# Performance work log

Hardware: AMD Instinct MI355X
Metric: run time of the kernel (lower is better)

The kernel has to match this reference:

```python
import jax, jax.numpy as jnp
import numpy as np

B, H, W, C = 32, 256, 256, 3
KH, KW, F = 5, 5, 8


def setup_inputs() -> dict:
    key = jax.random.key(0)
    k1, k2 = jax.random.split(key)
    x = jax.random.normal(k1, (B, H, W, C), dtype=jnp.float32)
    # learned structuring elements, shape (KH, KW, C, F) per build()
    kernel = jax.random.normal(k2, (KH, KW, C, F), dtype=jnp.float32) * 0.1
    return {"x": x, "kernel": kernel}


def _max_of_erosions(x, kernel):
    # tf.nn.erosion2d semantics: out[b,y,x,c] = min_{dy,dx} in[b, y+dy-pt, x+dx-pl, c]
    #                                               - kernel[KH-1-dy, KW-1-dx, c]
    # (erosion = -dilation(-x, reversed kernel)); then channel-max per filter.
    Bq, Hq, Wq, Cq = x.shape
    kh, kw, _, nf = kernel.shape
    pad_h, pad_w = kh - 1, kw - 1          # stride 1, rate 1, SAME padding
    pt, pl = pad_h // 2, pad_w // 2
    xp = jnp.pad(x, ((0, 0), (pt, pad_h - pt), (pl, pad_w - pl), (0, 0)),
                 constant_values=jnp.inf)   # +inf is identity for min
    kflip = kernel[::-1, ::-1]              # reflected structuring element
    ero = None                              # running min over window taps
    for dy in range(kh):                    # small fixed 5x5 tap loop
        for dx in range(kw):
            win = xp[:, dy:dy + Hq, dx:dx + Wq, :]          # [B,H,W,C]
            cand = win[..., None] - kflip[dy, dx]           # [B,H,W,C,F]
            ero = cand if ero is None else jnp.minimum(ero, cand)
    return jnp.max(ero, axis=3)             # channel max -> [B,H,W,F]


def reference(x, kernel):
    return _max_of_erosions(x, kernel)
```

## Files before the change

kernel.cpp:

```cpp
#include <hip/hip_runtime.h>
#include <math.h>


typedef _Float16 h2 __attribute__((ext_vector_type(2)));

static __device__ __forceinline__ h2 cvt_pk(float a, float b) {
    return __builtin_bit_cast(h2, __builtin_amdgcn_cvt_pkrtz(a, b));
}

#define Bq 32
#define Hq 256
#define Wq 256
#define Cq 3
#define NF 8

__global__ __launch_bounds__(256) void maxero_f16(
    const float* __restrict__ x,
    const float* __restrict__ kern,
    float* __restrict__ out)
{
    __shared__ h2 klds[25 * 12];
    for (int i = threadIdx.x; i < 300; i += 256) {
        int tap = i / 12;
        int rem = i - tap * 12;
        int c  = rem >> 2;
        int fp = rem & 3;
        int dy = tap / 5, dx = tap - dy * 5;
        const float* kp = kern + (((4 - dy) * 5 + (4 - dx)) * (Cq * NF)) + c * NF + fp * 2;
        klds[i] = cvt_pk(kp[0], kp[1]);
    }
    __syncthreads();

    const int idx  = blockIdx.x * 256 + threadIdx.x;
    const int pix0 = idx * 4;
    const int w0 = pix0 & (Wq - 1);
    const int h  = (pix0 >> 8) & (Hq - 1);
    const int b  = pix0 >> 16;

    const _Float16 HINF = (_Float16)__builtin_huge_valf();
    const h2 inf2 = { HINF, HINF };

    h2 ero[4][3][4];
    #pragma unroll
    for (int p = 0; p < 4; ++p)
        #pragma unroll
        for (int c = 0; c < 3; ++c)
            #pragma unroll
            for (int fp = 0; fp < 4; ++fp)
                ero[p][c][fp] = inf2;

    const float* xb = x + (size_t)b * (Hq * Wq * Cq);

    #pragma unroll
    for (int dy = 0; dy < 5; ++dy) {
        int r = h + dy - 2;
        bool rin = (unsigned)r < (unsigned)Hq;
        int rc = min(max(r, 0), Hq - 1);
        const float* rowp = xb + rc * (Wq * Cq);

        h2 xq[8][3];
        #pragma unroll
        for (int j = 0; j < 8; ++j) {
            int ccol = w0 - 2 + j;
            bool vin = rin && ((unsigned)ccol < (unsigned)Wq);
            int ccl = min(max(ccol, 0), Wq - 1);
            const float* p = rowp + ccl * 3;
            float v0 = p[0], v1 = p[1], v2 = p[2];
            h2 t0 = cvt_pk(v0, v0);
            h2 t1 = cvt_pk(v1, v1);
            h2 t2 = cvt_pk(v2, v2);
            xq[j][0] = vin ? t0 : inf2;
            xq[j][1] = vin ? t1 : inf2;
            xq[j][2] = vin ? t2 : inf2;
        }

        #pragma unroll
        for (int dx = 0; dx < 5; ++dx) {
            const h2* kk = &klds[(dy * 5 + dx) * 12];
            h2 kr[12];
            #pragma unroll
            for (int t = 0; t < 12; ++t) kr[t] = kk[t];
            #pragma unroll
            for (int p = 0; p < 4; ++p) {
                #pragma unroll
                for (int c = 0; c < 3; ++c) {
                    #pragma unroll
                    for (int fp = 0; fp < 4; ++fp) {
                        h2 cand = xq[p + dx][c] - kr[c * 4 + fp];
                        ero[p][c][fp] = __builtin_elementwise_min(ero[p][c][fp], cand);
                    }
                }
            }
        }
    }

    #pragma unroll
    for (int p = 0; p < 4; ++p) {
        float of[8];
        #pragma unroll
        for (int fp = 0; fp < 4; ++fp) {
            h2 m = __builtin_elementwise_max(
                       __builtin_elementwise_max(ero[p][0][fp], ero[p][1][fp]),
                       ero[p][2][fp]);
            of[fp * 2 + 0] = (float)m[0];
            of[fp * 2 + 1] = (float)m[1];
        }
        float* op = out + (size_t)(pix0 + p) * NF;
        reinterpret_cast<float4*>(op)[0] = make_float4(of[0], of[1], of[2], of[3]);
        reinterpret_cast<float4*>(op)[1] = make_float4(of[4], of[5], of[6], of[7]);
    }
}

extern "C" void kernel_launch(void* const* d_in, const int* in_sizes, int n_in,
                              void* d_out, int out_size, void* d_ws, size_t ws_size,
                              hipStream_t stream) {
    const float* x    = (const float*)d_in[0];
    const float* kern = (const float*)d_in[1];
    float* out        = (float*)d_out;
    const int threads = (Bq * Hq * Wq) / 4;
    maxero_f16<<<threads / 256, 256, 0, stream>>>(x, kern, out);
}
```

Baseline: 57.70 us.

## Stage input halo tile in LDS as packed f16 and read via vector loads

Each block now covers 4 output rows of one image. It loads the 8-row halo tile cooperatively with float4 global loads, converts it to packed f16 once, and stores it in LDS with inf padding. Threads then read their window rows as 128-bit LDS loads instead of issuing many scalar, clamped global loads and conversions per tap row. Kernel taps are also read as uint4. This trades the redundant global traffic and per-thread conversion work for LDS use (about 25KB per block) and a barrier, which may limit occupancy.

```diff
diff --git a/kernel.cpp b/kernel.cpp
--- a/kernel.cpp
+++ b/kernel.cpp
@@ -7,38 +7,66 @@
 static __device__ __forceinline__ h2 cvt_pk(float a, float b) {
     return __builtin_bit_cast(h2, __builtin_amdgcn_cvt_pkrtz(a, b));
 }
+static __device__ __forceinline__ h2 u2h(unsigned u) {
+    return __builtin_bit_cast(h2, u);
+}
 
 #define Bq 32
 #define Hq 256
 #define Wq 256
-#define Cq 3
-#define NF 8
 
-__global__ __launch_bounds__(256) void maxero_f16(
+#define RSTR 792
+#define TILE_H2 (8 * RSTR)
+
+#define INF2 0x7C007C00u
+
+__global__ __launch_bounds__(256) void maxero_lds(
     const float* __restrict__ x,
     const float* __restrict__ kern,
     float* __restrict__ out)
 {
+    __shared__ h2 xlds[TILE_H2];
     __shared__ h2 klds[25 * 12];
-    for (int i = threadIdx.x; i < 300; i += 256) {
+
+    const int tid = threadIdx.x;
+    const int bI  = blockIdx.x;
+    const int b   = bI >> 6;
+    const int h0  = (bI & 63) << 2;
+
+    for (int i = tid; i < 300; i += 256) {
         int tap = i / 12;
         int rem = i - tap * 12;
-        int c  = rem >> 2;
-        int fp = rem & 3;
+        int c = rem >> 2, fp = rem & 3;
         int dy = tap / 5, dx = tap - dy * 5;
-        const float* kp = kern + (((4 - dy) * 5 + (4 - dx)) * (Cq * NF)) + c * NF + fp * 2;
+        const float* kp = kern + (((4 - dy) * 5 + (4 - dx)) * 24) + c * 8 + fp * 2;
         klds[i] = cvt_pk(kp[0], kp[1]);
+    }
+
+    const float* xb = x + (size_t)b * (Hq * Wq * 3);
+    #pragma unroll
+    for (int k = 0; k < 6; ++k) {
+        int chunk = tid + k * 256;
+        int rr    = chunk / 192;
+        int off   = (chunk - rr * 192) * 4;
+        int r     = h0 - 2 + rr;
+        bool rv   = (unsigned)r < (unsigned)Hq;
+        int rc    = min(max(r, 0), Hq - 1);
+        const float4 v = *reinterpret_cast<const float4*>(xb + rc * 768 + off);
+        h2* d = &xlds[rr * RSTR + 18 + off];
+        d[0] = rv ? cvt_pk(v.x, v.x) : u2h(INF2);
+        d[1] = rv ? cvt_pk(v.y, v.y) : u2h(INF2);
+        d[2] = rv ? cvt_pk(v.z, v.z) : u2h(INF2);
+        d[3] = rv ? cvt_pk(v.w, v.w) : u2h(INF2);
+    }
+    if (tid < 192) {
+        int rr = tid / 24, p = tid - rr * 24;
+        int idx = rr * RSTR + (p < 18 ? p : 768 + p);
+        xlds[idx] = u2h(INF2);
     }
     __syncthreads();
 
-    const int idx  = blockIdx.x * 256 + threadIdx.x;
-    const int pix0 = idx * 4;
-    const int w0 = pix0 & (Wq - 1);
-    const int h  = (pix0 >> 8) & (Hq - 1);
-    const int b  = pix0 >> 16;
-
-    const _Float16 HINF = (_Float16)__builtin_huge_valf();
-    const h2 inf2 = { HINF, HINF };
+    const int hrow = tid >> 6;
+    const int w0   = (tid & 63) << 2;
 
     h2 ero[4][3][4];
     #pragma unroll
@@ -47,50 +75,32 @@
         for (int c = 0; c < 3; ++c)
             #pragma unroll
             for (int fp = 0; fp < 4; ++fp)
-                ero[p][c][fp] = inf2;
-
-    const float* xb = x + (size_t)b * (Hq * Wq * Cq);
+                ero[p][c][fp] = u2h(INF2);
 
     #pragma unroll
     for (int dy = 0; dy < 5; ++dy) {
-        int r = h + dy - 2;
-        bool rin = (unsigned)r < (unsigned)Hq;
-        int rc = min(max(r, 0), Hq - 1);
-        const float* rowp = xb + rc * (Wq * Cq);
-
-        h2 xq[8][3];
-        #pragma unroll
-        for (int j = 0; j < 8; ++j) {
-            int ccol = w0 - 2 + j;
-            bool vin = rin && ((unsigned)ccol < (unsigned)Wq);
-            int ccl = min(max(ccol, 0), Wq - 1);
-            const float* p = rowp + ccl * 3;
-            float v0 = p[0], v1 = p[1], v2 = p[2];
-            h2 t0 = cvt_pk(v0, v0);
-            h2 t1 = cvt_pk(v1, v1);
-            h2 t2 = cvt_pk(v2, v2);
-            xq[j][0] = vin ? t0 : inf2;
-            xq[j][1] = vin ? t1 : inf2;
-            xq[j][2] = vin ? t2 : inf2;
-        }
-
+        const uint4* rp = reinterpret_cast<const uint4*>(
+            &xlds[(hrow + dy) * RSTR + 12 + 3 * w0]);
+        uint4 q0 = rp[0], q1 = rp[1], q2 = rp[2], q3 = rp[3], q4 = rp[4], q5 = rp[5];
+        const unsigned qf[24] = { q0.x,q0.y,q0.z,q0.w, q1.x,q1.y,q1.z,q1.w,
+                                  q2.x,q2.y,q2.z,q2.w, q3.x,q3.y,q3.z,q3.w,
+                                  q4.x,q4.y,q4.z,q4.w, q5.x,q5.y,q5.z,q5.w };
         #pragma unroll
         for (int dx = 0; dx < 5; ++dx) {
-            const h2* kk = &klds[(dy * 5 + dx) * 12];
-            h2 kr[12];
+            const uint4* kk = reinterpret_cast<const uint4*>(&klds[(dy * 5 + dx) * 12]);
+            uint4 k0 = kk[0], k1 = kk[1], k2 = kk[2];
+            const unsigned kf[12] = { k0.x,k0.y,k0.z,k0.w,
+                                      k1.x,k1.y,k1.z,k1.w,
+                                      k2.x,k2.y,k2.z,k2.w };
             #pragma unroll
-            for (int t = 0; t < 12; ++t) kr[t] = kk[t];
-            #pragma unroll
-            for (int p = 0; p < 4; ++p) {
+            for (int p = 0; p < 4; ++p)
                 #pragma unroll
-                for (int c = 0; c < 3; ++c) {
+                for (int c = 0; c < 3; ++c)
                     #pragma unroll
                     for (int fp = 0; fp < 4; ++fp) {
-                        h2 cand = xq[p + dx][c] - kr[c * 4 + fp];
+                        h2 cand = u2h(qf[(p + dx) * 3 + c]) - u2h(kf[c * 4 + fp]);
                         ero[p][c][fp] = __builtin_elementwise_min(ero[p][c][fp], cand);
                     }
-                }
-            }
         }
     }
 
@@ -105,7 +115,8 @@
             of[fp * 2 + 0] = (float)m[0];
             of[fp * 2 + 1] = (float)m[1];
         }
-        float* op = out + (size_t)(pix0 + p) * NF;
+        size_t opix = ((size_t)b * 65536 + (size_t)(h0 + hrow) * 256 + (w0 + p));
+        float* op = out + opix * 8;
         reinterpret_cast<float4*>(op)[0] = make_float4(of[0], of[1], of[2], of[3]);
         reinterpret_cast<float4*>(op)[1] = make_float4(of[4], of[5], of[6], of[7]);
     }
@@ -117,6 +128,5 @@
     const float* x    = (const float*)d_in[0];
     const float* kern = (const float*)d_in[1];
     float* out        = (float*)d_out;
-    const int threads = (Bq * Hq * Wq) / 4;
-    maxero_f16<<<threads / 256, 256, 0, stream>>>(x, kern, out);
+    maxero_lds<<<2048, 256, 0, stream>>>(x, kern, out);
 }
```

After: 55.69 us. 3.5% less time.
